# Performance work log

Hardware: AMD Instinct MI355X
Metric: run time of the kernel (lower is better)

## Reference

```python
import jax, jax.numpy as jnp
import numpy as np

L, B, N, IN, H, ATTN, RED, OUT = 3, 8, 512, 64, 128, 32, 32, 3


def setup_inputs() -> dict:
    key = jax.random.key(0)
    ks = jax.random.split(key, 34)
    def rn(i, shape, s=0.05):
        return jax.random.normal(ks[i], shape, dtype=jnp.float32) * s
    inp = {
        "X": rn(0, (B, N, IN), 1.0),
        # sparse binary adjacency (avg degree ~10) and denser clique graph
        "A": (jax.random.uniform(ks[1], (B, N, N)) < 0.02).astype(jnp.float32),
        "Ac": (jax.random.uniform(ks[2], (B, N, N)) < 0.05).astype(jnp.float32),
        # topo embedding
        "embed_w": rn(3, (H, IN)), "embed_b": jnp.zeros((H,), jnp.float32),
        "topo_eps": jnp.zeros((1,), jnp.float32),
        "topo_w": rn(4, (H, H)), "topo_b": jnp.zeros((H,), jnp.float32),
        "theta": rn(5, (H, 2)),
        # per-layer dual GIN (index 0: A, index 1: Ac)
        "gin_eps": jnp.zeros((L, 2, 1), jnp.float32),
        "gin_w": rn(6, (L, 2, H, H)), "gin_b": jnp.zeros((L, 2, H), jnp.float32),
        # per-layer flexible attention
        "wo": rn(7, (L, ATTN, H)), "w1": rn(8, (L, ATTN, H)),
        "wphi": rn(9, (L, ATTN)),
        "wy_w": rn(10, (L, H, H)), "wy_b": jnp.zeros((L, H), jnp.float32),
        "we_w": rn(11, (L, H, ATTN)), "we_b": jnp.zeros((L, H), jnp.float32),
        # per-layer SE block
        "lin1_w": rn(12, (L, RED, H)), "lin1_b": jnp.zeros((L, RED), jnp.float32),
        "lin2_w": rn(13, (L, H, RED)), "lin2_b": jnp.zeros((L, H), jnp.float32),
        "mlp_w": rn(14, (L, H, H)), "mlp_b": jnp.zeros((L, H), jnp.float32),
        # node head
        "head1_w": rn(15, (H // 2, H)), "head1_b": jnp.zeros((H // 2,), jnp.float32),
        "head2_w": rn(16, (OUT, H // 2)), "head2_b": jnp.zeros((OUT,), jnp.float32),
    }
    return inp


def _lin(x, w, b=None):
    y = x @ w.T
    return y if b is None else y + b


def _gin(x, a, eps, w, b):
    # (1+eps)*X + A@X, then Linear, then ReLU
    return jax.nn.relu(_lin((1.0 + eps) * x + a @ x, w, b))


def _forward(X, A, Ac, embed_w, embed_b, topo_eps, topo_w, topo_b, theta,
             gin_eps, gin_w, gin_b, wo, w1, wphi, wy_w, wy_b, we_w, we_b,
             lin1_w, lin1_b, lin2_w, lin2_b, mlp_w, mlp_b,
             head1_w, head1_b, head2_w, head2_b):
    # TopoPositionalEmbedding (shared GIN on both graphs)
    Xh = _lin(X, embed_w, embed_b)                      # (B,N,H)
    hA = _gin(Xh, A, topo_eps[0], topo_w, topo_b)
    hAC = _gin(Xh, Ac, topo_eps[0], topo_w, topo_b)
    Xp = Xh + jnp.tanh(hA * theta[:, 0]) + jnp.tanh(hAC * theta[:, 1])

    for l in range(L):
        # dual GIN
        XA = _gin(Xp, A, gin_eps[l, 0, 0], gin_w[l, 0], gin_b[l, 0])
        XAC = _gin(Xp, Ac, gin_eps[l, 1, 0], gin_w[l, 1], gin_b[l, 1])
        # GRIT-style flexible attention
        ho = Xp @ wo[l].T                               # (B,N,ATTN)
        h1 = Xp @ w1[l].T
        e = jnp.tanh(ho[:, :, None, :] + h1[:, None, :, :])   # (B,N,N,ATTN)
        alpha = jax.nn.softmax(e @ wphi[l], axis=-1)    # (B,N,N)
        Xy = _lin(Xp, wy_w[l], wy_b[l])                 # (B,N,H)
        # sum_j alpha_ij * We(e_ij) == We(sum_j alpha_ij * e_ij) since We is affine
        # and sum_j alpha_ij == 1 (avoids the (B,N,N,H) intermediate)
        ctx = jnp.einsum('bij,bijd->bid', alpha, e)     # (B,N,ATTN)
        Xatt = alpha @ Xy + _lin(ctx, we_w[l], we_b[l])
        Xbar = XA + XAC + Xatt
        # SE gating
        y1 = jax.nn.relu(_lin(Xbar.sum(axis=1), lin1_w[l], lin1_b[l]))
        y2 = jax.nn.sigmoid(_lin(y1, lin2_w[l], lin2_b[l]))
        Xp = _lin(Xbar * y2[:, None, :], mlp_w[l], mlp_b[l])

    h = jax.nn.relu(_lin(Xp, head1_w, head1_b))
    return _lin(h, head2_w, head2_b)                    # (B,N,OUT)


def reference(X, A, Ac, embed_w, embed_b, topo_eps, topo_w, topo_b, theta,
              gin_eps, gin_w, gin_b, wo, w1, wphi, wy_w, wy_b, we_w, we_b,
              lin1_w, lin1_b, lin2_w, lin2_b, mlp_w, mlp_b,
              head1_w, head1_b, head2_w, head2_b):
    return _forward(X, A, Ac, embed_w, embed_b, topo_eps, topo_w, topo_b, theta,
                    gin_eps, gin_w, gin_b, wo, w1, wphi, wy_w, wy_b, we_w, we_b,
                    lin1_w, lin1_b, lin2_w, lin2_b, mlp_w, mlp_b,
                    head1_w, head1_b, head2_w, head2_b)
```

## Files before the change

### kernel.cpp

```cpp
#include <hip/hip_runtime.h>

#define Bc 8
#define Nc 512
#define INc 64
#define Hc 128
#define Atc 32
#define REDc 32
#define OUTc 3
#define Lc 3
#define MNc (Bc * Nc)
#define KT 32
#define WPAD 36

__device__ __forceinline__ float tanh_fast(float x) {
    float e = __expf(2.f * x);
    return 1.f - 2.f * __builtin_amdgcn_rcpf(e + 1.f);
}

__global__ __launch_bounds__(256) void prologue(
        const float* __restrict__ A, const float* __restrict__ Acg,
        int* __restrict__ idxA, int* __restrict__ idxC,
        int* __restrict__ cntA, int* __restrict__ cntC,
        const float* __restrict__ X, const float* __restrict__ embed_w,
        const float* __restrict__ embed_b, float* __restrict__ Xh) {
    __shared__ int cA, cC;
    __shared__ float xs[8 * INc];
    int blk = blockIdx.x;
    int t = threadIdx.x;
    if (blk < MNc) {
        if (t == 0) { cA = 0; cC = 0; }
        __syncthreads();
        if (t < 128) {
            int h = t;
            int* ia = idxA + (size_t)blk * Nc;
            int* ic = idxC + (size_t)blk * Nc;
            float4 a4 = ((const float4*)(A + (size_t)blk * Nc))[h];
            if (a4.x != 0.f) ia[atomicAdd(&cA, 1)] = 4 * h;
            if (a4.y != 0.f) ia[atomicAdd(&cA, 1)] = 4 * h + 1;
            if (a4.z != 0.f) ia[atomicAdd(&cA, 1)] = 4 * h + 2;
            if (a4.w != 0.f) ia[atomicAdd(&cA, 1)] = 4 * h + 3;
            float4 c4 = ((const float4*)(Acg + (size_t)blk * Nc))[h];
            if (c4.x != 0.f) ic[atomicAdd(&cC, 1)] = 4 * h;
            if (c4.y != 0.f) ic[atomicAdd(&cC, 1)] = 4 * h + 1;
            if (c4.z != 0.f) ic[atomicAdd(&cC, 1)] = 4 * h + 2;
            if (c4.w != 0.f) ic[atomicAdd(&cC, 1)] = 4 * h + 3;
        }
        __syncthreads();
        if (t == 0) { cntA[blk] = cA; cntC[blk] = cC; }
    } else {
        int m0 = (blk - MNc) * 8;
        if (t < 128) ((float4*)xs)[t] = ((const float4*)(X + (size_t)m0 * INc))[t];
        __syncthreads();
        int n = t & 127, grp = t >> 7;
        float bv = embed_b[n];
        float acc[4];
#pragma unroll
        for (int r = 0; r < 4; ++r) acc[r] = bv;
        const float* w = embed_w + (size_t)n * INc;
        for (int k = 0; k < INc; k += 4) {
            float4 wv = *(const float4*)(w + k);
#pragma unroll
            for (int r = 0; r < 4; ++r) {
                float4 xv = *(const float4*)(xs + (grp * 4 + r) * INc + k);
                acc[r] = fmaf(xv.x, wv.x, acc[r]); acc[r] = fmaf(xv.y, wv.y, acc[r]);
                acc[r] = fmaf(xv.z, wv.z, acc[r]); acc[r] = fmaf(xv.w, wv.w, acc[r]);
            }
        }
#pragma unroll
        for (int r = 0; r < 4; ++r)
            Xh[(size_t)(m0 + grp * 4 + r) * Hc + n] = acc[r];
    }
}

__global__ __launch_bounds__(128) void spmm_pre(
        const int* __restrict__ idxA, const int* __restrict__ idxC,
        const int* __restrict__ cntA, const int* __restrict__ cntC,
        const float* __restrict__ X, const float* __restrict__ eA,
        const float* __restrict__ eC, float* __restrict__ T1, float* __restrict__ T2) {
    int bi = blockIdx.x;
    int b = bi >> 9;
    int h = threadIdx.x;
    __shared__ int ias[Nc], ics[Nc];
    int nA = cntA[bi], nC = cntC[bi];
    for (int q = h; q < nA; q += 128) ias[q] = idxA[(size_t)bi * Nc + q];
    for (int q = h; q < nC; q += 128) ics[q] = idxC[(size_t)bi * Nc + q];
    __syncthreads();
    const float* Xb = X + (size_t)b * Nc * Hc;
    float a1 = 0.f, a2 = 0.f;
    for (int q = 0; q < nA; ++q) a1 += Xb[(size_t)ias[q] * Hc + h];
    for (int q = 0; q < nC; ++q) a2 += Xb[(size_t)ics[q] * Hc + h];
    size_t o = (size_t)bi * Hc + h;
    float xv = X[o];
    T1[o] = (1.f + eA[0]) * xv + a1;
    T2[o] = (1.f + eC[0]) * xv + a2;
}

__global__ __launch_bounds__(256) void gemm2_topo(
        const float* __restrict__ T1, const float* __restrict__ T2,
        const float* __restrict__ W, const float* __restrict__ bias,
        const float* __restrict__ Xh, const float* __restrict__ theta,
        float* __restrict__ Xp) {
    __shared__ float xs1[8 * Hc], xs2[8 * Hc];
    int m0 = blockIdx.x * 8;
    int t = threadIdx.x;
    for (int idx4 = t; idx4 < 8 * Hc / 4; idx4 += 256) {
        ((float4*)xs1)[idx4] = ((const float4*)(T1 + (size_t)m0 * Hc))[idx4];
        ((float4*)xs2)[idx4] = ((const float4*)(T2 + (size_t)m0 * Hc))[idx4];
    }
    __syncthreads();
    int n = t & 127, grp = t >> 7;
    float bv = bias[n];
    float ac1[4], ac2[4];
#pragma unroll
    for (int r = 0; r < 4; ++r) { ac1[r] = bv; ac2[r] = bv; }
    const float* w = W + (size_t)n * Hc;
    for (int k = 0; k < Hc; k += 4) {
        float4 wv = *(const float4*)(w + k);
#pragma unroll
        for (int r = 0; r < 4; ++r) {
            float4 x1 = *(const float4*)(xs1 + (grp * 4 + r) * Hc + k);
            float4 x2 = *(const float4*)(xs2 + (grp * 4 + r) * Hc + k);
            ac1[r] = fmaf(x1.x, wv.x, ac1[r]); ac1[r] = fmaf(x1.y, wv.y, ac1[r]);
            ac1[r] = fmaf(x1.z, wv.z, ac1[r]); ac1[r] = fmaf(x1.w, wv.w, ac1[r]);
            ac2[r] = fmaf(x2.x, wv.x, ac2[r]); ac2[r] = fmaf(x2.y, wv.y, ac2[r]);
            ac2[r] = fmaf(x2.z, wv.z, ac2[r]); ac2[r] = fmaf(x2.w, wv.w, ac2[r]);
        }
    }
    float th0 = theta[2 * n], th1 = theta[2 * n + 1];
#pragma unroll
    for (int r = 0; r < 4; ++r) {
        size_t o = (size_t)(m0 + grp * 4 + r) * Hc + n;
        float g1 = fmaxf(ac1[r], 0.f), g2 = fmaxf(ac2[r], 0.f);
        Xp[o] = Xh[o] + tanh_fast(g1 * th0) + tanh_fast(g2 * th1);
    }
}

__device__ __forceinline__ void stage_wtile(
        const float* __restrict__ W, int kt, float* Ws, int t) {
#pragma unroll
    for (int i = 0; i < 4; ++i) {
        int idx = t + i * 256;
        int row = idx >> 3, c4 = idx & 7;
        float4 v = *(const float4*)(W + (size_t)row * Hc + kt + c4 * 4);
        *(float4*)(Ws + row * WPAD + c4 * 4) = v;
    }
}

__device__ __forceinline__ void gemm_lds(
        const float* __restrict__ W, const float* xsrc, float* Ws,
        int n, int grp, int t, float acc[4]) {
#pragma unroll 1
    for (int kt = 0; kt < Hc; kt += KT) {
        __syncthreads();
        stage_wtile(W, kt, Ws, t);
        __syncthreads();
#pragma unroll
        for (int k = 0; k < KT; k += 4) {
            float4 wv = *(const float4*)(Ws + n * WPAD + k);
#pragma unroll
            for (int r = 0; r < 4; ++r) {
                float4 xv = *(const float4*)(xsrc + (grp * 4 + r) * Hc + kt + k);
                acc[r] = fmaf(xv.x, wv.x, acc[r]); acc[r] = fmaf(xv.y, wv.y, acc[r]);
                acc[r] = fmaf(xv.z, wv.z, acc[r]); acc[r] = fmaf(xv.w, wv.w, acc[r]);
            }
        }
    }
}

__global__ __launch_bounds__(256) void layer_gemm4(
        const float* __restrict__ T1, const float* __restrict__ T2,
        const float* __restrict__ W1, const float* __restrict__ b1,
        const float* __restrict__ W2, const float* __restrict__ b2,
        const float* __restrict__ Xp, const float* __restrict__ wy_w,
        const float* __restrict__ wy_b, const float* __restrict__ wo,
        const float* __restrict__ w1a, float* __restrict__ GS1,
        float* __restrict__ GS2, float* __restrict__ Xy,
        float* __restrict__ hov, float* __restrict__ h1v) {
    __shared__ float xs[32 * Hc];
    __shared__ float Ws[Hc * WPAD];
    int blk = blockIdx.x;
    int role = blk >> 7;
    int m0 = (blk & 127) * 32;
    int t = threadIdx.x;
    const float* xsrc = (role == 0) ? T1 : (role == 1) ? T2 : Xp;
    {
        const float4* src = (const float4*)(xsrc + (size_t)m0 * Hc);
#pragma unroll
        for (int i = 0; i < 4; ++i) ((float4*)xs)[t + i * 256] = src[t + i * 256];
    }
    if (role == 3) {
        __syncthreads();
        int n2 = t & 63, g2 = t >> 6;
        const float* w = (n2 < 32) ? (wo + (size_t)n2 * Hc) : (w1a + (size_t)(n2 - 32) * Hc);
        float acc[8];
#pragma unroll
        for (int r = 0; r < 8; ++r) acc[r] = 0.f;
        for (int k = 0; k < Hc; k += 4) {
            float4 wv = *(const float4*)(w + k);
#pragma unroll
            for (int r = 0; r < 8; ++r) {
                float4 xv = *(const float4*)(xs + (g2 * 8 + r) * Hc + k);
                acc[r] = fmaf(xv.x, wv.x, acc[r]); acc[r] = fmaf(xv.y, wv.y, acc[r]);
                acc[r] = fmaf(xv.z, wv.z, acc[r]); acc[r] = fmaf(xv.w, wv.w, acc[r]);
            }
        }
#pragma unroll
        for (int r = 0; r < 8; ++r) {
            int m = m0 + g2 * 8 + r;
            float v = tanh_fast(acc[r]);
            if (n2 < 32) hov[(size_t)m * Atc + n2] = v;
            else h1v[(size_t)m * Atc + (n2 - 32)] = v;
        }
        return;
    }
    const float* W = (role == 0) ? W1 : (role == 1) ? W2 : wy_w;
    const float* bias = (role == 0) ? b1 : (role == 1) ? b2 : wy_b;
    int cg = t & 31, rg = t >> 5;
    float acc[4][4];
#pragma unroll
    for (int r = 0; r < 4; ++r)
#pragma unroll
        for (int c = 0; c < 4; ++c) acc[r][c] = 0.f;
#pragma unroll 1
    for (int kt = 0; kt < Hc; kt += KT) {
        __syncthreads();
        stage_wtile(W, kt, Ws, t);
        __syncthreads();
#pragma unroll
        for (int k = 0; k < KT; k += 4) {
            float4 xv[4], wv[4];
#pragma unroll
            for (int r = 0; r < 4; ++r)
                xv[r] = *(const float4*)(xs + (rg * 4 + r) * Hc + kt + k);
#pragma unroll
            for (int c = 0; c < 4; ++c)
                wv[c] = *(const float4*)(Ws + (cg + 32 * c) * WPAD + k);
#pragma unroll
            for (int r = 0; r < 4; ++r)
#pragma unroll
                for (int c = 0; c < 4; ++c) {
                    acc[r][c] = fmaf(xv[r].x, wv[c].x, acc[r][c]);
                    acc[r][c] = fmaf(xv[r].y, wv[c].y, acc[r][c]);
                    acc[r][c] = fmaf(xv[r].z, wv[c].z, acc[r][c]);
                    acc[r][c] = fmaf(xv[r].w, wv[c].w, acc[r][c]);
                }
        }
    }
    float bvv[4];
#pragma unroll
    for (int c = 0; c < 4; ++c) bvv[c] = bias[cg + 32 * c];
    if (role == 0) {
#pragma unroll
        for (int r = 0; r < 4; ++r)
#pragma unroll
            for (int c = 0; c < 4; ++c)
                GS1[(size_t)(m0 + rg * 4 + r) * Hc + cg + 32 * c] =
                    fmaxf(acc[r][c] + bvv[c], 0.f);
    } else if (role == 1) {
#pragma unroll
        for (int r = 0; r < 4; ++r)
#pragma unroll
            for (int c = 0; c < 4; ++c)
                GS2[(size_t)(m0 + rg * 4 + r) * Hc + cg + 32 * c] =
                    fmaxf(acc[r][c] + bvv[c], 0.f);
    } else {
#pragma unroll
        for (int r = 0; r < 4; ++r)
#pragma unroll
            for (int c = 0; c < 4; ++c)
                Xy[(size_t)(m0 + rg * 4 + r) * Hc + cg + 32 * c] = acc[r][c] + bvv[c];
    }
}

__global__ __launch_bounds__(256, 4) void attn_part(
        const float* __restrict__ ta, const float* __restrict__ tb,
        const float* __restrict__ wphi, const float* __restrict__ Xy,
        float* __restrict__ Pp, float* __restrict__ ctxp, float* __restrict__ wsp) {
    int blk = blockIdx.x;
    int b = blk >> 8;
    int r6 = (blk >> 2) & 63;
    int js = blk & 3;
    int i0 = r6 * 8;
    int t = threadIdx.x;
    __shared__ float als[8 * 128];
    __shared__ float4 red4[1024];
    __shared__ float tas[8 * 32];
    tas[t] = ta[((size_t)b * Nc + i0) * 32 + t];
    __syncthreads();
    {
        int i = t >> 5;
        int kq = t & 3;
        int jl = (t >> 2) & 7;
        float4 wp0 = ((const float4*)wphi)[kq * 2];
        float4 wp1 = ((const float4*)wphi)[kq * 2 + 1];
        float4 ta0 = *(const float4*)(tas + i * 32 + kq * 8);
        float4 ta1 = *(const float4*)(tas + i * 32 + kq * 8 + 4);
        const float* tbb = tb + ((size_t)b * Nc + js * 128) * 32;
        const float4* p = (const float4*)(tbb + (size_t)jl * 32 + kq * 8);
        float4 c0a = p[0], c0b = p[1];
        float4 c1a = p[64], c1b = p[65];
        float ca[8];
#pragma unroll
        for (int q = 0; q < 8; ++q) ca[q] = 0.f;
        float wsum = 0.f;
#pragma unroll 4
        for (int jj = 0; jj < 16; ++jj) {
            float4 ha = c0a, hb = c0b;
            c0a = c1a; c0b = c1b;
            if (jj < 14) { c1a = p[(jj + 2) * 64]; c1b = p[(jj + 2) * 64 + 1]; }
            float e0 = (ta0.x + ha.x) * __builtin_amdgcn_rcpf(fmaf(ta0.x, ha.x, 1.f));
            float e1 = (ta0.y + ha.y) * __builtin_amdgcn_rcpf(fmaf(ta0.y, ha.y, 1.f));
            float e2 = (ta0.z + ha.z) * __builtin_amdgcn_rcpf(fmaf(ta0.z, ha.z, 1.f));
            float e3 = (ta0.w + ha.w) * __builtin_amdgcn_rcpf(fmaf(ta0.w, ha.w, 1.f));
            float e4 = (ta1.x + hb.x) * __builtin_amdgcn_rcpf(fmaf(ta1.x, hb.x, 1.f));
            float e5 = (ta1.y + hb.y) * __builtin_amdgcn_rcpf(fmaf(ta1.y, hb.y, 1.f));
            float e6 = (ta1.z + hb.z) * __builtin_amdgcn_rcpf(fmaf(ta1.z, hb.z, 1.f));
            float e7 = (ta1.w + hb.w) * __builtin_amdgcn_rcpf(fmaf(ta1.w, hb.w, 1.f));
            float s01 = fmaf(e1, wp0.y, e0 * wp0.x);
            float s23 = fmaf(e3, wp0.w, e2 * wp0.z);
            float s45 = fmaf(e5, wp1.y, e4 * wp1.x);
            float s67 = fmaf(e7, wp1.w, e6 * wp1.z);
            float sc = (s01 + s23) + (s45 + s67);
            sc += __shfl_xor(sc, 1);
            sc += __shfl_xor(sc, 2);
            float w = __expf(sc);
            if (kq == 0) als[i * 128 + jj * 8 + jl] = w;
            wsum += w;
            ca[0] = fmaf(w, e0, ca[0]);
            ca[1] = fmaf(w, e1, ca[1]);
            ca[2] = fmaf(w, e2, ca[2]);
            ca[3] = fmaf(w, e3, ca[3]);
            ca[4] = fmaf(w, e4, ca[4]);
            ca[5] = fmaf(w, e5, ca[5]);
            ca[6] = fmaf(w, e6, ca[6]);
            ca[7] = fmaf(w, e7, ca[7]);
        }
#pragma unroll
        for (int o = 16; o > 0; o >>= 1) wsum += __shfl_xor(wsum, o);
        if ((t & 31) == 0) wsp[(size_t)js * MNc + (size_t)b * Nc + i0 + i] = wsum;
#pragma unroll
        for (int q = 0; q < 8; ++q) {
            ca[q] += __shfl_xor(ca[q], 4);
            ca[q] += __shfl_xor(ca[q], 8);
            ca[q] += __shfl_xor(ca[q], 16);
        }
        if (jl == 0) {
            float* cp = ctxp + ((size_t)js * MNc + (size_t)b * Nc + i0 + i) * 32 + kq * 8;
#pragma unroll
            for (int q = 0; q < 8; ++q) cp[q] = ca[q];
        }
    }
    __syncthreads();
    {
        int h4 = t & 31, jg = t >> 5;
        const float* xp = Xy + (((size_t)b * Nc + js * 128) + jg * 16) * Hc + h4 * 4;
        float* Pb = Pp + (size_t)js * MNc * Hc;
        float4 acc[8];
#pragma unroll
        for (int r = 0; r < 8; ++r) acc[r] = make_float4(0.f, 0.f, 0.f, 0.f);
        float4 xc = *(const float4*)(xp);
        float4 xn = *(const float4*)(xp + Hc);
#pragma unroll 4
        for (int jq = 0; jq < 16; ++jq) {
            float4 x = xc;
            xc = xn;
            if (jq < 14) xn = *(const float4*)(xp + (jq + 2) * Hc);
            int j = jg * 16 + jq;
#pragma unroll
            for (int r = 0; r < 8; ++r) {
                float av = als[r * 128 + j];
                acc[r].x = fmaf(av, x.x, acc[r].x);
                acc[r].y = fmaf(av, x.y, acc[r].y);
                acc[r].z = fmaf(av, x.z, acc[r].z);
                acc[r].w = fmaf(av, x.w, acc[r].w);
            }
        }
#pragma unroll
        for (int r = 0; r < 4; ++r) red4[jg * 128 + r * 32 + h4] = acc[r];
        __syncthreads();
        if (t < 128) {
            int ii = t >> 5, hq = t & 31;
            float4 s = red4[ii * 32 + hq];
#pragma unroll
            for (int gq = 1; gq < 8; ++gq) {
                float4 p = red4[gq * 128 + ii * 32 + hq];
                s.x += p.x; s.y += p.y; s.z += p.z; s.w += p.w;
            }
            *(float4*)(Pb + ((size_t)b * Nc + i0 + ii) * Hc + hq * 4) = s;
        }
        __syncthreads();
#pragma unroll
        for (int r = 0; r < 4; ++r) red4[jg * 128 + r * 32 + h4] = acc[4 + r];
        __syncthreads();
        if (t < 128) {
            int ii = t >> 5, hq = t & 31;
            float4 s = red4[ii * 32 + hq];
#pragma unroll
            for (int gq = 1; gq < 8; ++gq) {
                float4 p = red4[gq * 128 + ii * 32 + hq];
                s.x += p.x; s.y += p.y; s.z += p.z; s.w += p.w;
            }
            *(float4*)(Pb + ((size_t)b * Nc + i0 + 4 + ii) * Hc + hq * 4) = s;
        }
    }
}

__global__ __launch_bounds__(256) void combine_se(
        const float* __restrict__ Pp, const float* __restrict__ ctxp,
        const float* __restrict__ wsp, const float* __restrict__ we_w,
        const float* __restrict__ we_b, const float* __restrict__ GS1,
        const float* __restrict__ GS2,
        float* __restrict__ Xbar, float* __restrict__ part) {
    int blk = blockIdx.x;
    int m0 = blk * 8;
    int t = threadIdx.x;
    __shared__ float ctxs[8 * 32];
    __shared__ float sinv[8];
    __shared__ float4 sred[256];
    if (t < 8) {
        float ws = 0.f;
#pragma unroll
        for (int s = 0; s < 4; ++s) ws += wsp[(size_t)s * MNc + m0 + t];
        sinv[t] = 4.f / ws;
    }
    {
        float c = 0.f;
#pragma unroll
        for (int s = 0; s < 4; ++s) c += ctxp[((size_t)s * MNc + m0) * 32 + t];
        ctxs[t] = c;
    }
    __syncthreads();
    int ii = t >> 5, hq = t & 31;
    size_t o = (size_t)(m0 + ii) * Hc + hq * 4;
    float4 ps = *(const float4*)(Pp + o);
#pragma unroll
    for (int s = 1; s < 4; ++s) {
        float4 p = *(const float4*)(Pp + (size_t)s * MNc * Hc + o);
        ps.x += p.x; ps.y += p.y; ps.z += p.z; ps.w += p.w;
    }
    float si = sinv[ii];
    const float* c = ctxs + ii * 32;
    float wec[4];
#pragma unroll
    for (int ho_ = 0; ho_ < 4; ++ho_) {
        const float4* wrow = (const float4*)(we_w + (size_t)(hq * 4 + ho_) * 32);
        float sv = 0.f;
#pragma unroll
        for (int q = 0; q < 8; ++q) {
            float4 w4 = wrow[q];
            sv = fmaf(w4.x, c[4 * q], sv); sv = fmaf(w4.y, c[4 * q + 1], sv);
            sv = fmaf(w4.z, c[4 * q + 2], sv); sv = fmaf(w4.w, c[4 * q + 3], sv);
        }
        wec[ho_] = sv;
    }
    float4 wb = *(const float4*)(we_b + hq * 4);
    float4 g1 = *(const float4*)(GS1 + o);
    float4 g2 = *(const float4*)(GS2 + o);
    float4 outv;
    outv.x = (ps.x + wec[0]) * si + wb.x + g1.x + g2.x;
    outv.y = (ps.y + wec[1]) * si + wb.y + g1.y + g2.y;
    outv.z = (ps.z + wec[2]) * si + wb.z + g1.z + g2.z;
    outv.w = (ps.w + wec[3]) * si + wb.w + g1.w + g2.w;
    *(float4*)(Xbar + o) = outv;
    sred[ii * 32 + hq] = outv;
    __syncthreads();
    if (t < 32) {
        float4 s0 = sred[t];
#pragma unroll
        for (int g = 1; g < 8; ++g) {
            float4 p = sred[g * 32 + t];
            s0.x += p.x; s0.y += p.y; s0.z += p.z; s0.w += p.w;
        }
        *(float4*)(part + (size_t)blk * Hc + t * 4) = s0;
    }
}

template <int LAST>
__global__ __launch_bounds__(256) void mlp_gemm(
        const float* __restrict__ Xbar, const float* __restrict__ W,
        const float* __restrict__ bias, const float* __restrict__ part,
        const float* __restrict__ l1w, const float* __restrict__ l1b,
        const float* __restrict__ l2w, const float* __restrict__ l2b,
        float* __restrict__ Y,
        const float* __restrict__ h1w, const float* __restrict__ h1b,
        const float* __restrict__ h2w, const float* __restrict__ h2b,
        float* __restrict__ out) {
    __shared__ float xs[8 * Hc];
    __shared__ float s[Hc];
    __shared__ float y1s[REDc];
    __shared__ float y2s[Hc];
    __shared__ float hs[8 * 64];
    __shared__ float Ws[Hc * WPAD];
    int m0 = blockIdx.x * 8;
    int b = m0 >> 9;
    int t = threadIdx.x;
    ((float4*)xs)[t] = ((const float4*)(Xbar + (size_t)m0 * Hc))[t];
    if (t < 128) {
        const float* pb = part + (size_t)b * 64 * Hc;
        float acc = 0.f;
        for (int p = 0; p < 64; ++p) acc += pb[p * Hc + t];
        s[t] = acc;
    }
    __syncthreads();
    if (t < REDc) {
        float a = l1b[t];
        const float* w = l1w + (size_t)t * Hc;
        for (int k = 0; k < Hc; ++k) a = fmaf(s[k], w[k], a);
        y1s[t] = fmaxf(a, 0.f);
    }
    __syncthreads();
    if (t < 128) {
        float a = l2b[t];
        const float* w2 = l2w + (size_t)t * REDc;
#pragma unroll
        for (int k = 0; k < REDc; ++k) a = fmaf(y1s[k], w2[k], a);
        y2s[t] = 1.f / (1.f + __expf(-a));
    }
    __syncthreads();
    {
        float4 yv = ((const float4*)y2s)[t & 31];
        float4 v = ((float4*)xs)[t];
        v.x *= yv.x; v.y *= yv.y; v.z *= yv.z; v.w *= yv.w;
        ((float4*)xs)[t] = v;
    }
    int n = t & 127, grp = t >> 7;
    float bv = bias[n];
    float acc[4];
#pragma unroll
    for (int r = 0; r < 4; ++r) acc[r] = bv;
    gemm_lds(W, xs, Ws, n, grp, t, acc);
    if (!LAST) {
#pragma unroll
        for (int r = 0; r < 4; ++r)
            Y[(size_t)(m0 + grp * 4 + r) * Hc + n] = acc[r];
    } else {
        __syncthreads();
#pragma unroll
        for (int r = 0; r < 4; ++r) xs[(grp * 4 + r) * Hc + n] = acc[r];
        __syncthreads();
        {
            int n2 = t & 63, g2 = t >> 6;
            float a0 = h1b[n2], a1 = a0;
            const float* wh = h1w + (size_t)n2 * Hc;
            const float* x0 = xs + (g2 * 2) * Hc;
            const float* x1 = xs + (g2 * 2 + 1) * Hc;
            for (int k = 0; k < Hc; k += 4) {
                float4 wv = *(const float4*)(wh + k);
                float4 v0 = *(const float4*)(x0 + k);
                float4 v1 = *(const float4*)(x1 + k);
                a0 = fmaf(v0.x, wv.x, a0); a0 = fmaf(v0.y, wv.y, a0);
                a0 = fmaf(v0.z, wv.z, a0); a0 = fmaf(v0.w, wv.w, a0);
                a1 = fmaf(v1.x, wv.x, a1); a1 = fmaf(v1.y, wv.y, a1);
                a1 = fmaf(v1.z, wv.z, a1); a1 = fmaf(v1.w, wv.w, a1);
            }
            hs[(g2 * 2) * 64 + n2] = fmaxf(a0, 0.f);
            hs[(g2 * 2 + 1) * 64 + n2] = fmaxf(a1, 0.f);
        }
        __syncthreads();
        if (t < 8 * OUTc) {
            int m = t / OUTc, o = t - m * OUTc;
            float a = h2b[o];
            const float* w2 = h2w + (size_t)o * 64;
            const float* hr = hs + m * 64;
#pragma unroll
            for (int k = 0; k < 64; ++k) a = fmaf(hr[k], w2[k], a);
            out[(size_t)(m0 + m) * OUTc + o] = a;
        }
    }
}

extern "C" void kernel_launch(void* const* d_in, const int* in_sizes, int n_in,
                              void* d_out, int out_size, void* d_ws, size_t ws_size,
                              hipStream_t stream) {
    const float* X       = (const float*)d_in[0];
    const float* A       = (const float*)d_in[1];
    const float* Acg     = (const float*)d_in[2];
    const float* embed_w = (const float*)d_in[3];
    const float* embed_b = (const float*)d_in[4];
    const float* topo_eps= (const float*)d_in[5];
    const float* topo_w  = (const float*)d_in[6];
    const float* topo_b  = (const float*)d_in[7];
    const float* theta   = (const float*)d_in[8];
    const float* gin_eps = (const float*)d_in[9];
    const float* gin_w   = (const float*)d_in[10];
    const float* gin_b   = (const float*)d_in[11];
    const float* wo      = (const float*)d_in[12];
    const float* w1      = (const float*)d_in[13];
    const float* wphi    = (const float*)d_in[14];
    const float* wy_w    = (const float*)d_in[15];
    const float* wy_b    = (const float*)d_in[16];
    const float* we_w    = (const float*)d_in[17];
    const float* we_b    = (const float*)d_in[18];
    const float* lin1_w  = (const float*)d_in[19];
    const float* lin1_b  = (const float*)d_in[20];
    const float* lin2_w  = (const float*)d_in[21];
    const float* lin2_b  = (const float*)d_in[22];
    const float* mlp_w   = (const float*)d_in[23];
    const float* mlp_b   = (const float*)d_in[24];
    const float* head1_w = (const float*)d_in[25];
    const float* head1_b = (const float*)d_in[26];
    const float* head2_w = (const float*)d_in[27];
    const float* head2_b = (const float*)d_in[28];
    float* out = (float*)d_out;

    float* ws = (float*)d_ws;
    const int MN = Bc * Nc;
    const size_t SZ = (size_t)MN * Hc;
    float* Xh   = ws;
    float* Xp   = Xh + SZ;
    float* T1   = Xp + SZ;
    float* T2   = T1 + SZ;
    float* GS1  = T2 + SZ;
    float* GS2  = GS1 + SZ;
    float* Xy   = GS2 + SZ;
    float* hov  = Xy + SZ;
    float* h1v  = hov + (size_t)MN * Atc;
    float* part = h1v + (size_t)MN * Atc;
    float* Pp   = part + (size_t)(MN / 8) * Hc;
    float* ctxp = Pp + 4 * SZ;
    float* wsp  = ctxp + (size_t)4 * MN * Atc;
    int* idxA   = (int*)(wsp + (size_t)4 * MN);
    int* idxC   = idxA + (size_t)MN * Nc;
    int* cntA   = idxC + (size_t)MN * Nc;
    int* cntC   = cntA + MN;
    float* Xbar = T1;

    prologue<<<MN + MN / 8, 256, 0, stream>>>(A, Acg, idxA, idxC, cntA, cntC,
                                              X, embed_w, embed_b, Xh);
    spmm_pre<<<MN, 128, 0, stream>>>(idxA, idxC, cntA, cntC, Xh, topo_eps, topo_eps, T1, T2);
    gemm2_topo<<<MN / 8, 256, 0, stream>>>(T1, T2, topo_w, topo_b, Xh, theta, Xp);

    for (int l = 0; l < Lc; ++l) {
        spmm_pre<<<MN, 128, 0, stream>>>(idxA, idxC, cntA, cntC, Xp,
                                         gin_eps + l * 2, gin_eps + l * 2 + 1, T1, T2);
        layer_gemm4<<<4 * (MN / 32), 256, 0, stream>>>(T1, T2,
            gin_w + (size_t)(l * 2 + 0) * Hc * Hc, gin_b + (size_t)(l * 2 + 0) * Hc,
            gin_w + (size_t)(l * 2 + 1) * Hc * Hc, gin_b + (size_t)(l * 2 + 1) * Hc,
            Xp, wy_w + (size_t)l * Hc * Hc, wy_b + (size_t)l * Hc,
            wo + (size_t)l * Atc * Hc, w1 + (size_t)l * Atc * Hc,
            GS1, GS2, Xy, hov, h1v);
        attn_part<<<MN / 2, 256, 0, stream>>>(hov, h1v, wphi + (size_t)l * Atc, Xy,
                                              Pp, ctxp, wsp);
        combine_se<<<MN / 8, 256, 0, stream>>>(Pp, ctxp, wsp,
                                               we_w + (size_t)l * Hc * Atc,
                                               we_b + (size_t)l * Hc, GS1, GS2, Xbar, part);
        if (l < Lc - 1) {
            mlp_gemm<0><<<MN / 8, 256, 0, stream>>>(Xbar, mlp_w + (size_t)l * Hc * Hc,
                mlp_b + (size_t)l * Hc, part,
                lin1_w + (size_t)l * REDc * Hc, lin1_b + (size_t)l * REDc,
                lin2_w + (size_t)l * Hc * REDc, lin2_b + (size_t)l * Hc,
                Xp, head1_w, head1_b, head2_w, head2_b, out);
        } else {
            mlp_gemm<1><<<MN / 8, 256, 0, stream>>>(Xbar, mlp_w + (size_t)l * Hc * Hc,
                mlp_b + (size_t)l * Hc, part,
                lin1_w + (size_t)l * REDc * Hc, lin1_b + (size_t)l * REDc,
                lin2_w + (size_t)l * Hc * REDc, lin2_b + (size_t)l * Hc,
                Xp, head1_w, head1_b, head2_w, head2_b, out);
        }
    }
}
```

Before: 376.2 us.

## Use 32-row register-tiled GEMMs for topo embedding and MLP kernels

Replaces the 8-row-per-block topo GEMM and MLP GEMM with 32-row blocks. Each thread now computes a 4x4 register tile with weights staged in LDS, so each weight load is reused across more rows. The change also cuts the number of SE reductions over the partial sums, since fewer blocks each redo them. In exchange there are 4x fewer blocks (128 in total), which lowers occupancy and GPU fill, raises register pressure, and uses more LDS per block.

```diff
diff --git a/kernel.cpp b/kernel.cpp
--- a/kernel.cpp
+++ b/kernel.cpp
@@ -95,46 +95,6 @@
     T2[o] = (1.f + eC[0]) * xv + a2;
 }
 
-__global__ __launch_bounds__(256) void gemm2_topo(
-        const float* __restrict__ T1, const float* __restrict__ T2,
-        const float* __restrict__ W, const float* __restrict__ bias,
-        const float* __restrict__ Xh, const float* __restrict__ theta,
-        float* __restrict__ Xp) {
-    __shared__ float xs1[8 * Hc], xs2[8 * Hc];
-    int m0 = blockIdx.x * 8;
-    int t = threadIdx.x;
-    for (int idx4 = t; idx4 < 8 * Hc / 4; idx4 += 256) {
-        ((float4*)xs1)[idx4] = ((const float4*)(T1 + (size_t)m0 * Hc))[idx4];
-        ((float4*)xs2)[idx4] = ((const float4*)(T2 + (size_t)m0 * Hc))[idx4];
-    }
-    __syncthreads();
-    int n = t & 127, grp = t >> 7;
-    float bv = bias[n];
-    float ac1[4], ac2[4];
-#pragma unroll
-    for (int r = 0; r < 4; ++r) { ac1[r] = bv; ac2[r] = bv; }
-    const float* w = W + (size_t)n * Hc;
-    for (int k = 0; k < Hc; k += 4) {
-        float4 wv = *(const float4*)(w + k);
-#pragma unroll
-        for (int r = 0; r < 4; ++r) {
-            float4 x1 = *(const float4*)(xs1 + (grp * 4 + r) * Hc + k);
-            float4 x2 = *(const float4*)(xs2 + (grp * 4 + r) * Hc + k);
-            ac1[r] = fmaf(x1.x, wv.x, ac1[r]); ac1[r] = fmaf(x1.y, wv.y, ac1[r]);
-            ac1[r] = fmaf(x1.z, wv.z, ac1[r]); ac1[r] = fmaf(x1.w, wv.w, ac1[r]);
-            ac2[r] = fmaf(x2.x, wv.x, ac2[r]); ac2[r] = fmaf(x2.y, wv.y, ac2[r]);
-            ac2[r] = fmaf(x2.z, wv.z, ac2[r]); ac2[r] = fmaf(x2.w, wv.w, ac2[r]);
-        }
-    }
-    float th0 = theta[2 * n], th1 = theta[2 * n + 1];
-#pragma unroll
-    for (int r = 0; r < 4; ++r) {
-        size_t o = (size_t)(m0 + grp * 4 + r) * Hc + n;
-        float g1 = fmaxf(ac1[r], 0.f), g2 = fmaxf(ac2[r], 0.f);
-        Xp[o] = Xh[o] + tanh_fast(g1 * th0) + tanh_fast(g2 * th1);
-    }
-}
-
 __device__ __forceinline__ void stage_wtile(
         const float* __restrict__ W, int kt, float* Ws, int t) {
 #pragma unroll
@@ -146,9 +106,31 @@
     }
 }
 
-__device__ __forceinline__ void gemm_lds(
-        const float* __restrict__ W, const float* xsrc, float* Ws,
-        int n, int grp, int t, float acc[4]) {
+__global__ __launch_bounds__(256) void topo_gemm4(
+        const float* __restrict__ T1, const float* __restrict__ T2,
+        const float* __restrict__ W, const float* __restrict__ bias,
+        const float* __restrict__ Xh, const float* __restrict__ theta,
+        float* __restrict__ Xp) {
+    __shared__ float xs1[32 * Hc];
+    __shared__ float xs2[32 * Hc];
+    __shared__ float Ws[Hc * WPAD];
+    int m0 = blockIdx.x * 32;
+    int t = threadIdx.x;
+    {
+        const float4* s1 = (const float4*)(T1 + (size_t)m0 * Hc);
+        const float4* s2 = (const float4*)(T2 + (size_t)m0 * Hc);
+#pragma unroll
+        for (int i = 0; i < 4; ++i) {
+            ((float4*)xs1)[t + i * 256] = s1[t + i * 256];
+            ((float4*)xs2)[t + i * 256] = s2[t + i * 256];
+        }
+    }
+    int cg = t & 31, rg = t >> 5;
+    float ac1[4][4], ac2[4][4];
+#pragma unroll
+    for (int r = 0; r < 4; ++r)
+#pragma unroll
+        for (int c = 0; c < 4; ++c) { ac1[r][c] = 0.f; ac2[r][c] = 0.f; }
 #pragma unroll 1
     for (int kt = 0; kt < Hc; kt += KT) {
         __syncthreads();
@@ -156,13 +138,41 @@
         __syncthreads();
 #pragma unroll
         for (int k = 0; k < KT; k += 4) {
-            float4 wv = *(const float4*)(Ws + n * WPAD + k);
+            float4 x1[4], x2[4], wv[4];
 #pragma unroll
             for (int r = 0; r < 4; ++r) {
-                float4 xv = *(const float4*)(xsrc + (grp * 4 + r) * Hc + kt + k);
-                acc[r] = fmaf(xv.x, wv.x, acc[r]); acc[r] = fmaf(xv.y, wv.y, acc[r]);
-                acc[r] = fmaf(xv.z, wv.z, acc[r]); acc[r] = fmaf(xv.w, wv.w, acc[r]);
+                x1[r] = *(const float4*)(xs1 + (rg * 4 + r) * Hc + kt + k);
+                x2[r] = *(const float4*)(xs2 + (rg * 4 + r) * Hc + kt + k);
             }
+#pragma unroll
+            for (int c = 0; c < 4; ++c)
+                wv[c] = *(const float4*)(Ws + (cg + 32 * c) * WPAD + k);
+#pragma unroll
+            for (int r = 0; r < 4; ++r)
+#pragma unroll
+                for (int c = 0; c < 4; ++c) {
+                    ac1[r][c] = fmaf(x1[r].x, wv[c].x, ac1[r][c]);
+                    ac1[r][c] = fmaf(x1[r].y, wv[c].y, ac1[r][c]);
+                    ac1[r][c] = fmaf(x1[r].z, wv[c].z, ac1[r][c]);
+                    ac1[r][c] = fmaf(x1[r].w, wv[c].w, ac1[r][c]);
+                    ac2[r][c] = fmaf(x2[r].x, wv[c].x, ac2[r][c]);
+                    ac2[r][c] = fmaf(x2[r].y, wv[c].y, ac2[r][c]);
+                    ac2[r][c] = fmaf(x2[r].z, wv[c].z, ac2[r][c]);
+                    ac2[r][c] = fmaf(x2[r].w, wv[c].w, ac2[r][c]);
+                }
+        }
+    }
+#pragma unroll
+    for (int c = 0; c < 4; ++c) {
+        int n = cg + 32 * c;
+        float bv = bias[n];
+        float th0 = theta[2 * n], th1 = theta[2 * n + 1];
+#pragma unroll
+        for (int r = 0; r < 4; ++r) {
+            size_t o = (size_t)(m0 + rg * 4 + r) * Hc + n;
+            float g1 = fmaxf(ac1[r][c] + bv, 0.f);
+            float g2 = fmaxf(ac2[r][c] + bv, 0.f);
+            Xp[o] = Xh[o] + tanh_fast(g1 * th0) + tanh_fast(g2 * th1);
         }
     }
 }
@@ -476,7 +486,7 @@
 }
 
 template <int LAST>
-__global__ __launch_bounds__(256) void mlp_gemm(
+__global__ __launch_bounds__(256) void mlp_gemm4(
         const float* __restrict__ Xbar, const float* __restrict__ W,
         const float* __restrict__ bias, const float* __restrict__ part,
         const float* __restrict__ l1w, const float* __restrict__ l1b,
@@ -485,16 +495,19 @@
         const float* __restrict__ h1w, const float* __restrict__ h1b,
         const float* __restrict__ h2w, const float* __restrict__ h2b,
         float* __restrict__ out) {
-    __shared__ float xs[8 * Hc];
+    __shared__ float xs[32 * Hc];
+    __shared__ float Ws[Hc * WPAD];
     __shared__ float s[Hc];
     __shared__ float y1s[REDc];
     __shared__ float y2s[Hc];
-    __shared__ float hs[8 * 64];
-    __shared__ float Ws[Hc * WPAD];
-    int m0 = blockIdx.x * 8;
+    int m0 = blockIdx.x * 32;
     int b = m0 >> 9;
     int t = threadIdx.x;
-    ((float4*)xs)[t] = ((const float4*)(Xbar + (size_t)m0 * Hc))[t];
+    {
+        const float4* src = (const float4*)(Xbar + (size_t)m0 * Hc);
+#pragma unroll
+        for (int i = 0; i < 4; ++i) ((float4*)xs)[t + i * 256] = src[t + i * 256];
+    }
     if (t < 128) {
         const float* pb = part + (size_t)b * 64 * Hc;
         float acc = 0.f;
@@ -518,46 +531,86 @@
     }
     __syncthreads();
     {
-        float4 yv = ((const float4*)y2s)[t & 31];
-        float4 v = ((float4*)xs)[t];
-        v.x *= yv.x; v.y *= yv.y; v.z *= yv.z; v.w *= yv.w;
-        ((float4*)xs)[t] = v;
-    }
-    int n = t & 127, grp = t >> 7;
-    float bv = bias[n];
-    float acc[4];
-#pragma unroll
-    for (int r = 0; r < 4; ++r) acc[r] = bv;
-    gemm_lds(W, xs, Ws, n, grp, t, acc);
+#pragma unroll
+        for (int i = 0; i < 4; ++i) {
+            int idx = t + i * 256;
+            float4 yv = ((const float4*)y2s)[idx & 31];
+            float4 v = ((float4*)xs)[idx];
+            v.x *= yv.x; v.y *= yv.y; v.z *= yv.z; v.w *= yv.w;
+            ((float4*)xs)[idx] = v;
+        }
+    }
+    int cg = t & 31, rg = t >> 5;
+    float acc[4][4];
+#pragma unroll
+    for (int r = 0; r < 4; ++r)
+#pragma unroll
+        for (int c = 0; c < 4; ++c) acc[r][c] = 0.f;
+#pragma unroll 1
+    for (int kt = 0; kt < Hc; kt += KT) {
+        __syncthreads();
+        stage_wtile(W, kt, Ws, t);
+        __syncthreads();
+#pragma unroll
+        for (int k = 0; k < KT; k += 4) {
+            float4 xv[4], wv[4];
+#pragma unroll
+            for (int r = 0; r < 4; ++r)
+                xv[r] = *(const float4*)(xs + (rg * 4 + r) * Hc + kt + k);
+#pragma unroll
+            for (int c = 0; c < 4; ++c)
+                wv[c] = *(const float4*)(Ws + (cg + 32 * c) * WPAD + k);
+#pragma unroll
+            for (int r = 0; r < 4; ++r)
+#pragma unroll
+                for (int c = 0; c < 4; ++c) {
+                    acc[r][c] = fmaf(xv[r].x, wv[c].x, acc[r][c]);
+                    acc[r][c] = fmaf(xv[r].y, wv[c].y, acc[r][c]);
+                    acc[r][c] = fmaf(xv[r].z, wv[c].z, acc[r][c]);
+                    acc[r][c] = fmaf(xv[r].w, wv[c].w, acc[r][c]);
+                }
+        }
+    }
+    float bvv[4];
+#pragma unroll
+    for (int c = 0; c < 4; ++c) bvv[c] = bias[cg + 32 * c];
     if (!LAST) {
 #pragma unroll
         for (int r = 0; r < 4; ++r)
-            Y[(size_t)(m0 + grp * 4 + r) * Hc + n] = acc[r];
+#pragma unroll
+            for (int c = 0; c < 4; ++c)
+                Y[(size_t)(m0 + rg * 4 + r) * Hc + cg + 32 * c] = acc[r][c] + bvv[c];
     } else {
-        __syncthreads();
-#pragma unroll
-        for (int r = 0; r < 4; ++r) xs[(grp * 4 + r) * Hc + n] = acc[r];
+        float* hs = Ws;
+        __syncthreads();
+#pragma unroll
+        for (int r = 0; r < 4; ++r)
+#pragma unroll
+            for (int c = 0; c < 4; ++c)
+                xs[(rg * 4 + r) * Hc + cg + 32 * c] = acc[r][c] + bvv[c];
         __syncthreads();
         {
             int n2 = t & 63, g2 = t >> 6;
-            float a0 = h1b[n2], a1 = a0;
+            float a[8];
             const float* wh = h1w + (size_t)n2 * Hc;
-            const float* x0 = xs + (g2 * 2) * Hc;
-            const float* x1 = xs + (g2 * 2 + 1) * Hc;
+            float bh = h1b[n2];
+#pragma unroll
+            for (int r = 0; r < 8; ++r) a[r] = bh;
             for (int k = 0; k < Hc; k += 4) {
                 float4 wv = *(const float4*)(wh + k);
-                float4 v0 = *(const float4*)(x0 + k);
-                float4 v1 = *(const float4*)(x1 + k);
-                a0 = fmaf(v0.x, wv.x, a0); a0 = fmaf(v0.y, wv.y, a0);
-                a0 = fmaf(v0.z, wv.z, a0); a0 = fmaf(v0.w, wv.w, a0);
-                a1 = fmaf(v1.x, wv.x, a1); a1 = fmaf(v1.y, wv.y, a1);
-                a1 = fmaf(v1.z, wv.z, a1); a1 = fmaf(v1.w, wv.w, a1);
+#pragma unroll
+                for (int r = 0; r < 8; ++r) {
+                    float4 xv = *(const float4*)(xs + (g2 * 8 + r) * Hc + k);
+                    a[r] = fmaf(xv.x, wv.x, a[r]); a[r] = fmaf(xv.y, wv.y, a[r]);
+                    a[r] = fmaf(xv.z, wv.z, a[r]); a[r] = fmaf(xv.w, wv.w, a[r]);
+                }
             }
-            hs[(g2 * 2) * 64 + n2] = fmaxf(a0, 0.f);
-            hs[(g2 * 2 + 1) * 64 + n2] = fmaxf(a1, 0.f);
-        }
-        __syncthreads();
-        if (t < 8 * OUTc) {
+#pragma unroll
+            for (int r = 0; r < 8; ++r)
+                hs[(g2 * 8 + r) * 64 + n2] = fmaxf(a[r], 0.f);
+        }
+        __syncthreads();
+        if (t < 32 * OUTc) {
             int m = t / OUTc, o = t - m * OUTc;
             float a = h2b[o];
             const float* w2 = h2w + (size_t)o * 64;
@@ -628,7 +681,7 @@
     prologue<<<MN + MN / 8, 256, 0, stream>>>(A, Acg, idxA, idxC, cntA, cntC,
                                               X, embed_w, embed_b, Xh);
     spmm_pre<<<MN, 128, 0, stream>>>(idxA, idxC, cntA, cntC, Xh, topo_eps, topo_eps, T1, T2);
-    gemm2_topo<<<MN / 8, 256, 0, stream>>>(T1, T2, topo_w, topo_b, Xh, theta, Xp);
+    topo_gemm4<<<MN / 32, 256, 0, stream>>>(T1, T2, topo_w, topo_b, Xh, theta, Xp);
 
     for (int l = 0; l < Lc; ++l) {
         spmm_pre<<<MN, 128, 0, stream>>>(idxA, idxC, cntA, cntC, Xp,
@@ -645,13 +698,13 @@
                                                we_w + (size_t)l * Hc * Atc,
                                                we_b + (size_t)l * Hc, GS1, GS2, Xbar, part);
         if (l < Lc - 1) {
-            mlp_gemm<0><<<MN / 8, 256, 0, stream>>>(Xbar, mlp_w + (size_t)l * Hc * Hc,
+            mlp_gemm4<0><<<MN / 32, 256, 0, stream>>>(Xbar, mlp_w + (size_t)l * Hc * Hc,
                 mlp_b + (size_t)l * Hc, part,
                 lin1_w + (size_t)l * REDc * Hc, lin1_b + (size_t)l * REDc,
                 lin2_w + (size_t)l * Hc * REDc, lin2_b + (size_t)l * Hc,
                 Xp, head1_w, head1_b, head2_w, head2_b, out);
         } else {
-            mlp_gemm<1><<<MN / 8, 256, 0, stream>>>(Xbar, mlp_w + (size_t)l * Hc * Hc,
+            mlp_gemm4<1><<<MN / 32, 256, 0, stream>>>(Xbar, mlp_w + (size_t)l * Hc * Hc,
                 mlp_b + (size_t)l * Hc, part,
                 lin1_w + (size_t)l * REDc * Hc, lin1_b + (size_t)l * REDc,
                 lin2_w + (size_t)l * Hc * REDc, lin2_b + (size_t)l * Hc,
```

Result: no change. 380.0 us (+1.0%).
